# Performance work log

Measured on AMD Instinct MI355X. Metric: run time of the kernel, lower is better.

The kernel has to match this reference:

```python
import jax, jax.numpy as jnp
import numpy as np

B, L, D = 2, 1024, 1024
H = 16
NL = 2
DFF = 4 * D
EPS = 1e-5
W_SCALE = 0.02


def rmsnorm(x, w):
    # x * rsqrt(mean(x^2, -1) + eps) * w   (computed in fp32 as in the torch code)
    xf = x.astype(jnp.float32)
    n = xf * jax.lax.rsqrt(jnp.mean(xf * xf, axis=-1, keepdims=True) + EPS)
    return n.astype(x.dtype) * w


def setup_inputs() -> dict:
    key = jax.random.key(0)
    ks = jax.random.split(key, 10)
    x = jax.random.normal(ks[0], (B, L, D), dtype=jnp.float32)
    # torch nn.Linear weight layout: [out_features, in_features]; y = x @ W.T + b
    qw = jax.random.normal(ks[1], (NL, D, D), dtype=jnp.float32) * W_SCALE
    kw = jax.random.normal(ks[2], (NL, D, D), dtype=jnp.float32) * W_SCALE
    vw = jax.random.normal(ks[3], (NL, D, D), dtype=jnp.float32) * W_SCALE
    ow = jax.random.normal(ks[4], (NL, D, D), dtype=jnp.float32) * W_SCALE
    pn_w = jnp.ones((NL, D), dtype=jnp.float32)
    ln_w = jnp.ones((NL, D), dtype=jnp.float32)
    fc_w = jax.random.normal(ks[5], (NL, DFF, D), dtype=jnp.float32) * W_SCALE
    fc2_w = jax.random.normal(ks[6], (NL, D, DFF), dtype=jnp.float32) * W_SCALE
    fc2_b = jnp.zeros((NL, D), dtype=jnp.float32)
    return {"x": x, "qw": qw, "kw": kw, "vw": vw, "ow": ow,
            "pn_w": pn_w, "ln_w": ln_w, "fc_w": fc_w, "fc2_w": fc2_w, "fc2_b": fc2_b}


def reference(x, qw, kw, vw, ow, pn_w, ln_w, fc_w, fc2_w, fc2_b):
    d = D // H
    for i in range(NL):
        # --- LinearAttention block (dropout=0 -> identity) ---
        h = rmsnorm(x, pn_w[i])                                   # [B,L,D]
        Q = (h @ qw[i].T).reshape(B, L, H, d)
        K = (h @ kw[i].T).reshape(B, L, H, d)
        V = (h @ vw[i].T).reshape(B, L, H, d)
        # outer-product state per position, cumulated over L (causal linear attn)
        W = jnp.einsum('blhd,blhe->blhde', K, V)                  # [B,L,H,d,d]
        W = jnp.cumsum(W, axis=1)
        a = jnp.einsum('blhd,blhde->blhe', Q, W).reshape(B, L, D)
        x = x + a @ ow[i].T
        # --- MLP block ---
        m = rmsnorm(x, ln_w[i])
        f = jax.nn.gelu(m @ fc_w[i].T, approximate=False)         # torch nn.GELU default = exact
        x = x + f @ fc2_w[i].T + fc2_b[i]
    return x
```

## Files before the change

kernel.cpp:

```cpp
#include <hip/hip_runtime.h>

#define BB 2
#define LL 1024
#define DD 1024
#define HH 16
#define HD 64
#define DFFN 4096
#define MM (BB*LL)
#define QS 3072

using u16 = unsigned short;
typedef __bf16 bf16x8 __attribute__((ext_vector_type(8)));
typedef float f32x4 __attribute__((ext_vector_type(4)));

__device__ __forceinline__ float b2f(u16 u) {
  union { unsigned int i; float f; } v; v.i = ((unsigned int)u) << 16; return v.f;
}
__device__ __forceinline__ u16 f2b(float f) {
  union { float f; unsigned int i; } v; v.f = f;
  unsigned int x = v.i;
  return (u16)((x + 0x7fffu + ((x >> 16) & 1u)) >> 16);
}
__device__ __forceinline__ float gelu_exact(float x) {
  return 0.5f * x * (1.0f + erff(x * 0.70710678118654752f));
}
__device__ __forceinline__ void gl2lds16(const void* g, void* l) {
  __builtin_amdgcn_global_load_lds((const __attribute__((address_space(1))) void*)g,
                                   (__attribute__((address_space(3))) void*)l, 16, 0, 0);
}

__global__ __launch_bounds__(256) void castw_kernel(const float* __restrict__ in,
                                                    u16* __restrict__ out, int n8) {
  int i = blockIdx.x * 256 + threadIdx.x;
  if (i >= n8) return;
  const float4 a = reinterpret_cast<const float4*>(in)[2 * i];
  const float4 b = reinterpret_cast<const float4*>(in)[2 * i + 1];
  uint4 o;
  o.x = (unsigned)f2b(a.x) | ((unsigned)f2b(a.y) << 16);
  o.y = (unsigned)f2b(a.z) | ((unsigned)f2b(a.w) << 16);
  o.z = (unsigned)f2b(b.x) | ((unsigned)f2b(b.y) << 16);
  o.w = (unsigned)f2b(b.z) | ((unsigned)f2b(b.w) << 16);
  reinterpret_cast<uint4*>(out)[i] = o;
}

__global__ __launch_bounds__(256) void rmsnorm_kernel(const float* __restrict__ x,
                                                      const float* __restrict__ w,
                                                      u16* __restrict__ out) {
  const int row = blockIdx.x, t = threadIdx.x;
  const float4 v = reinterpret_cast<const float4*>(x + (size_t)row * DD)[t];
  float ss = v.x*v.x + v.y*v.y + v.z*v.z + v.w*v.w;
  #pragma unroll
  for (int o = 32; o > 0; o >>= 1) ss += __shfl_down(ss, o);
  __shared__ float red[4];
  if ((t & 63) == 0) red[t >> 6] = ss;
  __syncthreads();
  const float inv = rsqrtf((red[0] + red[1] + red[2] + red[3]) * (1.0f / DD) + 1e-5f);
  const float4 wv = reinterpret_cast<const float4*>(w)[t];
  ushort4 o;
  o.x = f2b(v.x * inv * wv.x);
  o.y = f2b(v.y * inv * wv.y);
  o.z = f2b(v.z * inv * wv.z);
  o.w = f2b(v.w * inv * wv.w);
  reinterpret_cast<ushort4*>(out + (size_t)row * DD)[t] = o;
}

template<int BM, int BN, int ACT, int RES>
__global__ __launch_bounds__((BM/64)*(BN/64)*64)
void mfma_gemm(const u16* __restrict__ A, const u16* __restrict__ Wb,
               u16* __restrict__ Cb, const float* __restrict__ resid,
               float* __restrict__ Co, const float* __restrict__ bias,
               int N, int K) {
  constexpr int WCOLS = BN / 64;
  constexpr int NW = (BM / 64) * WCOLS;
  constexpr int NT = NW * 64;
  constexpr int CA = BM * 4;
  constexpr int CB = BN * 4;
  constexpr int IA = CA / NT, IB = CB / NT;
  __shared__ u16 As[BM * 32];
  __shared__ u16 Bs[BN * 32];
  const int t = threadIdx.x;
  const int lane = t & 63, w = t >> 6;
  const int wm = (w / WCOLS) * 64, wn = (w % WCOLS) * 64;
  const int m0 = blockIdx.y * BM, n0 = blockIdx.x * BN;
  const int fr = lane & 15, fq = lane >> 4;

  f32x4 acc[4][4] = {};

  for (int kt = 0; kt < K; kt += 32) {
    #pragma unroll
    for (int i = 0; i < IA; i++) {
      const int c = i * NT + t;
      gl2lds16(A + (size_t)(m0 + (c >> 2)) * K + kt + (c & 3) * 8, &As[c * 8]);
    }
    #pragma unroll
    for (int i = 0; i < IB; i++) {
      const int c = i * NT + t;
      gl2lds16(Wb + (size_t)(n0 + (c >> 2)) * K + kt + (c & 3) * 8, &Bs[c * 8]);
    }
    __syncthreads();
    bf16x8 af[4], bfv[4];
    #pragma unroll
    for (int i = 0; i < 4; i++)
      af[i] = *reinterpret_cast<const bf16x8*>(&As[(wm + i * 16 + fr) * 32 + fq * 8]);
    #pragma unroll
    for (int j = 0; j < 4; j++)
      bfv[j] = *reinterpret_cast<const bf16x8*>(&Bs[(wn + j * 16 + fr) * 32 + fq * 8]);
    #pragma unroll
    for (int i = 0; i < 4; i++)
      #pragma unroll
      for (int j = 0; j < 4; j++)
        acc[i][j] = __builtin_amdgcn_mfma_f32_16x16x32_bf16(af[i], bfv[j], acc[i][j], 0, 0, 0);
    __syncthreads();
  }

  #pragma unroll
  for (int i = 0; i < 4; i++) {
    #pragma unroll
    for (int j = 0; j < 4; j++) {
      #pragma unroll
      for (int r = 0; r < 4; r++) {
        const int row = m0 + wm + i * 16 + fq * 4 + r;
        const int col = n0 + wn + j * 16 + fr;
        float val = acc[i][j][r];
        if (RES == 0) {
          if (ACT == 1) val = gelu_exact(val);
          Cb[(size_t)row * N + col] = f2b(val);
        } else {
          const float rv = resid[(size_t)row * N + col];
          const float bv = (bias != nullptr) ? bias[col] : 0.0f;
          Co[(size_t)row * N + col] = rv + val + bv;
        }
      }
    }
  }
}

__global__ __launch_bounds__(256) void kv_trans(const u16* __restrict__ QKV,
                                                u16* __restrict__ Kt, u16* __restrict__ Vt) {
  const int tile = blockIdx.x;
  const int h2 = blockIdx.y;
  const int b = blockIdx.z;
  const int h = h2 & 15, which = h2 >> 4;
  const int t = threadIdx.x;
  const int pos = tile * 64 + (t >> 2), d0 = (t & 3) * 16;
  const u16* src = QKV + ((size_t)(b * LL) + pos) * QS + 1024 + which * 1024 + h * HD + d0;
  union { uint4 u[2]; u16 s[16]; } pk;
  pk.u[0] = reinterpret_cast<const uint4*>(src)[0];
  pk.u[1] = reinterpret_cast<const uint4*>(src)[1];
  u16* dst = (which ? Vt : Kt) + ((size_t)(b * HH + h) * HD + d0) * LL + pos;
  #pragma unroll
  for (int j = 0; j < 16; j++) dst[(size_t)j * LL] = pk.s[j];
}

__global__ __launch_bounds__(256) void attn_phase1(const u16* __restrict__ QKV,
                                                   const u16* __restrict__ Kt,
                                                   const u16* __restrict__ Vt,
                                                   u16* __restrict__ Oa,
                                                   u16* __restrict__ Slt) {
  __shared__ u16 Ss[4][16][64];
  const int tile = blockIdx.x, h = blockIdx.y, b = blockIdx.z;
  const int t = threadIdx.x, lane = t & 63, w = t >> 6;
  const int fr = lane & 15, fq = lane >> 4;
  const size_t tok0 = (size_t)(b * LL + tile * 64);
  const size_t bh = (size_t)(b * HH + h);
  const u16* Qb  = QKV + tok0 * QS + h * HD;
  const u16* Kb  = Qb + 1024;
  const u16* Ktb = Kt + bh * (HD * LL) + tile * 64;
  const u16* Vtb = Vt + bh * (HD * LL) + tile * 64;

  bf16x8 aq[2], bk[4][2];
  #pragma unroll
  for (int kh = 0; kh < 2; kh++)
    aq[kh] = *reinterpret_cast<const bf16x8*>(Qb + (size_t)(16*w + fr) * QS + kh*32 + fq*8);
  #pragma unroll
  for (int n4 = 0; n4 < 4; n4++)
    #pragma unroll
    for (int kh = 0; kh < 2; kh++)
      bk[n4][kh] = *reinterpret_cast<const bf16x8*>(Kb + (size_t)(16*n4 + fr) * QS + kh*32 + fq*8);
  f32x4 sacc[4] = {};
  #pragma unroll
  for (int n4 = 0; n4 < 4; n4++) {
    sacc[n4] = __builtin_amdgcn_mfma_f32_16x16x32_bf16(aq[0], bk[n4][0], sacc[n4], 0, 0, 0);
    sacc[n4] = __builtin_amdgcn_mfma_f32_16x16x32_bf16(aq[1], bk[n4][1], sacc[n4], 0, 0, 0);
  }
  #pragma unroll
  for (int n4 = 0; n4 < 4; n4++)
    #pragma unroll
    for (int r = 0; r < 4; r++) {
      const bool keep = (16*w + 4*fq + r) >= (16*n4 + fr);
      Ss[w][4*fq + r][16*n4 + fr] = keep ? f2b(sacc[n4][r]) : (u16)0;
    }
  __syncthreads();

  bf16x8 va[2], kt[4][2];
  #pragma unroll
  for (int kh = 0; kh < 2; kh++)
    va[kh] = *reinterpret_cast<const bf16x8*>(Vtb + (size_t)(16*w + fr) * LL + kh*32 + fq*8);
  #pragma unroll
  for (int n4 = 0; n4 < 4; n4++)
    #pragma unroll
    for (int kh = 0; kh < 2; kh++)
      kt[n4][kh] = *reinterpret_cast<const bf16x8*>(Ktb + (size_t)(16*n4 + fr) * LL + kh*32 + fq*8);
  f32x4 lacc[4] = {};
  #pragma unroll
  for (int n4 = 0; n4 < 4; n4++) {
    lacc[n4] = __builtin_amdgcn_mfma_f32_16x16x32_bf16(va[0], kt[n4][0], lacc[n4], 0, 0, 0);
    lacc[n4] = __builtin_amdgcn_mfma_f32_16x16x32_bf16(va[1], kt[n4][1], lacc[n4], 0, 0, 0);
  }
  u16* So = Slt + (bh * 16 + tile) * 4096;
  #pragma unroll
  for (int n4 = 0; n4 < 4; n4++)
    #pragma unroll
    for (int r = 0; r < 4; r++)
      So[(size_t)(16*w + 4*fq + r) * 64 + 16*n4 + fr] = f2b(lacc[n4][r]);

  bf16x8 sa[2], vb[4][2];
  #pragma unroll
  for (int kh = 0; kh < 2; kh++)
    sa[kh] = *reinterpret_cast<const bf16x8*>(&Ss[w][fr][kh*32 + fq*8]);
  #pragma unroll
  for (int n4 = 0; n4 < 4; n4++)
    #pragma unroll
    for (int kh = 0; kh < 2; kh++)
      vb[n4][kh] = *reinterpret_cast<const bf16x8*>(Vtb + (size_t)(16*n4 + fr) * LL + kh*32 + fq*8);
  f32x4 oacc[4] = {};
  #pragma unroll
  for (int n4 = 0; n4 < 4; n4++) {
    oacc[n4] = __builtin_amdgcn_mfma_f32_16x16x32_bf16(sa[0], vb[n4][0], oacc[n4], 0, 0, 0);
    oacc[n4] = __builtin_amdgcn_mfma_f32_16x16x32_bf16(sa[1], vb[n4][1], oacc[n4], 0, 0, 0);
  }
  u16* Ob = Oa + (tok0 + 16*w) * DD + h * HD;
  #pragma unroll
  for (int n4 = 0; n4 < 4; n4++)
    #pragma unroll
    for (int r = 0; r < 4; r++)
      Ob[(size_t)(4*fq + r) * DD + 16*n4 + fr] = f2b(oacc[n4][r]);
}

__global__ __launch_bounds__(256) void attn_phase2(const u16* __restrict__ Slt,
                                                   u16* __restrict__ Wc) {
  const int rg = blockIdx.x, h = blockIdx.y, b = blockIdx.z;
  const size_t base = ((size_t)((b * HH + h) * 16)) * 4096 + rg * 512 + threadIdx.x * 2;
  float r0 = 0.f, r1 = 0.f;
  for (int tl = 0; tl < 16; tl++) {
    const size_t p = base + (size_t)tl * 4096;
    const unsigned d = *reinterpret_cast<const unsigned*>(Slt + p);
    *reinterpret_cast<unsigned*>(Wc + p) = (unsigned)f2b(r0) | ((unsigned)f2b(r1) << 16);
    r0 += b2f((u16)(d & 0xffff));
    r1 += b2f((u16)(d >> 16));
  }
}

__global__ __launch_bounds__(256) void attn_phase3(const u16* __restrict__ QKV,
                                                   const u16* __restrict__ Wc,
                                                   u16* __restrict__ Oa) {
  const int tile = blockIdx.x, h = blockIdx.y, b = blockIdx.z;
  const int t = threadIdx.x, lane = t & 63, w = t >> 6;
  const int fr = lane & 15, fq = lane >> 4;
  const size_t tok0 = (size_t)(b * LL + tile * 64);
  const size_t bh = (size_t)(b * HH + h);
  const u16* Qb = QKV + tok0 * QS + h * HD;
  const u16* Wb = Wc + (bh * 16 + tile) * 4096;

  bf16x8 aq[2], wb[4][2];
  #pragma unroll
  for (int kh = 0; kh < 2; kh++)
    aq[kh] = *reinterpret_cast<const bf16x8*>(Qb + (size_t)(16*w + fr) * QS + kh*32 + fq*8);
  #pragma unroll
  for (int n4 = 0; n4 < 4; n4++)
    #pragma unroll
    for (int kh = 0; kh < 2; kh++)
      wb[n4][kh] = *reinterpret_cast<const bf16x8*>(Wb + (size_t)(16*n4 + fr) * 64 + kh*32 + fq*8);
  f32x4 oacc[4] = {};
  #pragma unroll
  for (int n4 = 0; n4 < 4; n4++) {
    oacc[n4] = __builtin_amdgcn_mfma_f32_16x16x32_bf16(aq[0], wb[n4][0], oacc[n4], 0, 0, 0);
    oacc[n4] = __builtin_amdgcn_mfma_f32_16x16x32_bf16(aq[1], wb[n4][1], oacc[n4], 0, 0, 0);
  }
  u16* Ob = Oa + (tok0 + 16*w) * DD + h * HD;
  #pragma unroll
  for (int n4 = 0; n4 < 4; n4++)
    #pragma unroll
    for (int r = 0; r < 4; r++) {
      const size_t idx = (size_t)(4*fq + r) * DD + 16*n4 + fr;
      Ob[idx] = f2b(b2f(Ob[idx]) + oacc[n4][r]);
    }
}

extern "C" void kernel_launch(void* const* d_in, const int* in_sizes, int n_in,
                              void* d_out, int out_size, void* d_ws, size_t ws_size,
                              hipStream_t stream) {
  const float* x_in = (const float*)d_in[0];
  const float* qw   = (const float*)d_in[1];
  const float* kw   = (const float*)d_in[2];
  const float* vw   = (const float*)d_in[3];
  const float* ow   = (const float*)d_in[4];
  const float* pn   = (const float*)d_in[5];
  const float* ln   = (const float*)d_in[6];
  const float* fcw  = (const float*)d_in[7];
  const float* fc2w = (const float*)d_in[8];
  const float* fc2b = (const float*)d_in[9];

  char* ws = (char*)d_ws;
  u16* wbuf = (u16*)ws;
  u16* slt  = (u16*)ws;
  u16* wcum = (u16*)(ws + (size_t)(4 << 20));
  u16* h    = (u16*)(ws + (size_t)(8 << 20));
  u16* qkv  = (u16*)(ws + (size_t)(12 << 20));
  u16* f    = (u16*)(ws + (size_t)(12 << 20));
  u16* vt   = (u16*)(ws + (size_t)(24 << 20));
  u16* kt   = (u16*)(ws + (size_t)(28 << 20));
  float* xf = (float*)d_out;

  const int n8D = DD * DD / 8;
  const int n8F = DFFN * DD / 8;

  for (int i = 0; i < 2; i++) {
    const float* qwi  = qw   + (size_t)i * DD * DD;
    const float* kwi  = kw   + (size_t)i * DD * DD;
    const float* vwi  = vw   + (size_t)i * DD * DD;
    const float* owi  = ow   + (size_t)i * DD * DD;
    const float* fcwi = fcw  + (size_t)i * DFFN * DD;
    const float* f2wi = fc2w + (size_t)i * DD * DFFN;
    const float* src  = (i == 0) ? x_in : xf;

    rmsnorm_kernel<<<MM, 256, 0, stream>>>(src, pn + i * DD, h);
    castw_kernel<<<n8D / 256, 256, 0, stream>>>(qwi, wbuf,               n8D);
    castw_kernel<<<n8D / 256, 256, 0, stream>>>(kwi, wbuf + DD * DD,     n8D);
    castw_kernel<<<n8D / 256, 256, 0, stream>>>(vwi, wbuf + 2 * DD * DD, n8D);
    mfma_gemm<128, 128, 0, 0><<<dim3(QS / 128, MM / 128), 256, 0, stream>>>(
        h, wbuf, qkv, nullptr, nullptr, nullptr, QS, DD);
    kv_trans<<<dim3(16, 32, BB), 256, 0, stream>>>(qkv, kt, vt);
    attn_phase1<<<dim3(16, HH, BB), 256, 0, stream>>>(qkv, kt, vt, h, slt);
    attn_phase2<<<dim3(8, HH, BB), 256, 0, stream>>>(slt, wcum);
    attn_phase3<<<dim3(16, HH, BB), 256, 0, stream>>>(qkv, wcum, h);
    castw_kernel<<<n8D / 256, 256, 0, stream>>>(owi, wbuf, n8D);
    mfma_gemm<64, 128, 0, 1><<<dim3(DD / 128, MM / 64), 128, 0, stream>>>(
        h, wbuf, nullptr, src, xf, nullptr, DD, DD);
    rmsnorm_kernel<<<MM, 256, 0, stream>>>(xf, ln + i * DD, h);
    castw_kernel<<<n8F / 256, 256, 0, stream>>>(fcwi, wbuf, n8F);
    mfma_gemm<128, 128, 1, 0><<<dim3(DFFN / 128, MM / 128), 256, 0, stream>>>(
        h, wbuf, f, nullptr, nullptr, nullptr, DFFN, DD);
    castw_kernel<<<n8F / 256, 256, 0, stream>>>(f2wi, wbuf, n8F);
    float* co = (i == 1) ? (float*)d_out : xf;
    mfma_gemm<64, 128, 0, 1><<<dim3(DD / 128, MM / 64), 128, 0, stream>>>(
        f, wbuf, nullptr, xf, co, fc2b + i * DD, DD, DFFN);
  }
}
```

Measured before the change: 607.1 us.

## Split-K residual GEMMs with atomics, fuse QKV weight casts, tile kv transpose

```diff
diff --git a/kernel.cpp b/kernel.cpp
--- a/kernel.cpp
+++ b/kernel.cpp
@@ -42,6 +42,35 @@
   o.w = (unsigned)f2b(b.z) | ((unsigned)f2b(b.w) << 16);
   reinterpret_cast<uint4*>(out)[i] = o;
 }
+__global__ __launch_bounds__(256) void castw3_kernel(const float* __restrict__ s0,
+                                                     const float* __restrict__ s1,
+                                                     const float* __restrict__ s2,
+                                                     u16* __restrict__ out, int n8) {
+  int i = blockIdx.x * 256 + threadIdx.x;
+  if (i >= n8) return;
+  const float* in = (blockIdx.y == 0) ? s0 : (blockIdx.y == 1) ? s1 : s2;
+  u16* dst = out + (size_t)blockIdx.y * n8 * 8;
+  const float4 a = reinterpret_cast<const float4*>(in)[2 * i];
+  const float4 b = reinterpret_cast<const float4*>(in)[2 * i + 1];
+  uint4 o;
+  o.x = (unsigned)f2b(a.x) | ((unsigned)f2b(a.y) << 16);
+  o.y = (unsigned)f2b(a.z) | ((unsigned)f2b(a.w) << 16);
+  o.z = (unsigned)f2b(b.x) | ((unsigned)f2b(b.y) << 16);
+  o.w = (unsigned)f2b(b.z) | ((unsigned)f2b(b.w) << 16);
+  reinterpret_cast<uint4*>(dst)[i] = o;
+}
+
+__global__ __launch_bounds__(256) void init_out_kernel(float* __restrict__ out,
+                                                       const float* __restrict__ resid,
+                                                       const float* __restrict__ bias) {
+  const int i = blockIdx.x * 256 + threadIdx.x;
+  float4 v = reinterpret_cast<const float4*>(resid)[i];
+  if (bias != nullptr) {
+    const float4 bv = *reinterpret_cast<const float4*>(bias + ((i * 4) & (DD - 1)));
+    v.x += bv.x; v.y += bv.y; v.z += bv.z; v.w += bv.w;
+  }
+  reinterpret_cast<float4*>(out)[i] = v;
+}
 
 __global__ __launch_bounds__(256) void rmsnorm_kernel(const float* __restrict__ x,
                                                       const float* __restrict__ w,
@@ -64,18 +93,14 @@
   reinterpret_cast<ushort4*>(out + (size_t)row * DD)[t] = o;
 }
 
-template<int BM, int BN, int ACT, int RES>
+template<int BM, int BN, int ACT>
 __global__ __launch_bounds__((BM/64)*(BN/64)*64)
 void mfma_gemm(const u16* __restrict__ A, const u16* __restrict__ Wb,
-               u16* __restrict__ Cb, const float* __restrict__ resid,
-               float* __restrict__ Co, const float* __restrict__ bias,
-               int N, int K) {
+               u16* __restrict__ Cb, int N, int K) {
   constexpr int WCOLS = BN / 64;
   constexpr int NW = (BM / 64) * WCOLS;
   constexpr int NT = NW * 64;
-  constexpr int CA = BM * 4;
-  constexpr int CB = BN * 4;
-  constexpr int IA = CA / NT, IB = CB / NT;
+  constexpr int IA = BM * 4 / NT, IB = BN * 4 / NT;
   __shared__ u16 As[BM * 32];
   __shared__ u16 Bs[BN * 32];
   const int t = threadIdx.x;
@@ -85,7 +110,6 @@
   const int fr = lane & 15, fq = lane >> 4;
 
   f32x4 acc[4][4] = {};
-
   for (int kt = 0; kt < K; kt += 32) {
     #pragma unroll
     for (int i = 0; i < IA; i++) {
@@ -114,42 +138,92 @@
   }
 
   #pragma unroll
-  for (int i = 0; i < 4; i++) {
-    #pragma unroll
-    for (int j = 0; j < 4; j++) {
+  for (int i = 0; i < 4; i++)
+    #pragma unroll
+    for (int j = 0; j < 4; j++)
       #pragma unroll
       for (int r = 0; r < 4; r++) {
         const int row = m0 + wm + i * 16 + fq * 4 + r;
         const int col = n0 + wn + j * 16 + fr;
         float val = acc[i][j][r];
-        if (RES == 0) {
-          if (ACT == 1) val = gelu_exact(val);
-          Cb[(size_t)row * N + col] = f2b(val);
-        } else {
-          const float rv = resid[(size_t)row * N + col];
-          const float bv = (bias != nullptr) ? bias[col] : 0.0f;
-          Co[(size_t)row * N + col] = rv + val + bv;
-        }
+        if (ACT == 1) val = gelu_exact(val);
+        Cb[(size_t)row * N + col] = f2b(val);
       }
+}
+
+template<int SPLIT>
+__global__ __launch_bounds__(256)
+void mfma_gemm_sk(const u16* __restrict__ A, const u16* __restrict__ Wb,
+                  float* __restrict__ Co, int N, int K) {
+  constexpr int BM = 128, BN = 128;
+  __shared__ u16 As[BM * 32];
+  __shared__ u16 Bs[BN * 32];
+  const int t = threadIdx.x;
+  const int lane = t & 63, w = t >> 6;
+  const int wm = (w >> 1) * 64, wn = (w & 1) * 64;
+  const int m0 = blockIdx.y * BM, n0 = blockIdx.x * BN;
+  const int fr = lane & 15, fq = lane >> 4;
+  const int Kc = K / SPLIT, k0 = blockIdx.z * Kc;
+
+  f32x4 acc[4][4] = {};
+  for (int kt = k0; kt < k0 + Kc; kt += 32) {
+    #pragma unroll
+    for (int i = 0; i < 2; i++) {
+      const int c = i * 256 + t;
+      gl2lds16(A + (size_t)(m0 + (c >> 2)) * K + kt + (c & 3) * 8, &As[c * 8]);
+      gl2lds16(Wb + (size_t)(n0 + (c >> 2)) * K + kt + (c & 3) * 8, &Bs[c * 8]);
     }
-  }
+    __syncthreads();
+    bf16x8 af[4], bfv[4];
+    #pragma unroll
+    for (int i = 0; i < 4; i++)
+      af[i] = *reinterpret_cast<const bf16x8*>(&As[(wm + i * 16 + fr) * 32 + fq * 8]);
+    #pragma unroll
+    for (int j = 0; j < 4; j++)
+      bfv[j] = *reinterpret_cast<const bf16x8*>(&Bs[(wn + j * 16 + fr) * 32 + fq * 8]);
+    #pragma unroll
+    for (int i = 0; i < 4; i++)
+      #pragma unroll
+      for (int j = 0; j < 4; j++)
+        acc[i][j] = __builtin_amdgcn_mfma_f32_16x16x32_bf16(af[i], bfv[j], acc[i][j], 0, 0, 0);
+    __syncthreads();
+  }
+
+  #pragma unroll
+  for (int i = 0; i < 4; i++)
+    #pragma unroll
+    for (int j = 0; j < 4; j++)
+      #pragma unroll
+      for (int r = 0; r < 4; r++) {
+        const int row = m0 + wm + i * 16 + fq * 4 + r;
+        const int col = n0 + wn + j * 16 + fr;
+        unsafeAtomicAdd(&Co[(size_t)row * N + col], acc[i][j][r]);
+      }
 }
 
 __global__ __launch_bounds__(256) void kv_trans(const u16* __restrict__ QKV,
                                                 u16* __restrict__ Kt, u16* __restrict__ Vt) {
+  __shared__ u16 T[64][72];
   const int tile = blockIdx.x;
   const int h2 = blockIdx.y;
   const int b = blockIdx.z;
   const int h = h2 & 15, which = h2 >> 4;
   const int t = threadIdx.x;
-  const int pos = tile * 64 + (t >> 2), d0 = (t & 3) * 16;
-  const u16* src = QKV + ((size_t)(b * LL) + pos) * QS + 1024 + which * 1024 + h * HD + d0;
+  const int pos = t >> 2, d0 = (t & 3) * 16;
+  const u16* src = QKV + ((size_t)(b * LL) + tile * 64 + pos) * QS + 1024 + which * 1024 + h * HD + d0;
   union { uint4 u[2]; u16 s[16]; } pk;
   pk.u[0] = reinterpret_cast<const uint4*>(src)[0];
   pk.u[1] = reinterpret_cast<const uint4*>(src)[1];
-  u16* dst = (which ? Vt : Kt) + ((size_t)(b * HH + h) * HD + d0) * LL + pos;
-  #pragma unroll
-  for (int j = 0; j < 16; j++) dst[(size_t)j * LL] = pk.s[j];
+  #pragma unroll
+  for (int j = 0; j < 16; j++) T[d0 + j][pos] = pk.s[j];
+  __syncthreads();
+  const int d = t >> 2, p0 = (t & 3) * 16;
+  u16* dst = (which ? Vt : Kt) + ((size_t)(b * HH + h) * HD + d) * LL + tile * 64 + p0;
+  union { uint4 u[2]; u16 s[16]; } ok;
+  #pragma unroll
+  for (int j = 0; j < 16; j++) ok.s[j] = T[d][p0 + j];
+  reinterpret_cast<uint4*>(dst)[0] = ok.u[0];
+  reinterpret_cast<uint4*>(dst)[1] = ok.u[1];
 }
 
 __global__ __launch_bounds__(256) void attn_phase1(const u16* __restrict__ QKV,
@@ -314,6 +388,7 @@
 
   const int n8D = DD * DD / 8;
   const int n8F = DFFN * DD / 8;
+  const int gInit = MM * DD / 4 / 256;
 
   for (int i = 0; i < 2; i++) {
     const float* qwi  = qw   + (size_t)i * DD * DD;
@@ -325,25 +400,23 @@
     const float* src  = (i == 0) ? x_in : xf;
 
     rmsnorm_kernel<<<MM, 256, 0, stream>>>(src, pn + i * DD, h);
-    castw_kernel<<<n8D / 256, 256, 0, stream>>>(qwi, wbuf,               n8D);
-    castw_kernel<<<n8D / 256, 256, 0, stream>>>(kwi, wbuf + DD * DD,     n8D);
-    castw_kernel<<<n8D / 256, 256, 0, stream>>>(vwi, wbuf + 2 * DD * DD, n8D);
-    mfma_gemm<128, 128, 0, 0><<<dim3(QS / 128, MM / 128), 256, 0, stream>>>(
-        h, wbuf, qkv, nullptr, nullptr, nullptr, QS, DD);
+    castw3_kernel<<<dim3(n8D / 256, 3), 256, 0, stream>>>(qwi, kwi, vwi, wbuf, n8D);
+    mfma_gemm<128, 128, 0><<<dim3(QS / 128, MM / 128), 256, 0, stream>>>(
+        h, wbuf, qkv, QS, DD);
     kv_trans<<<dim3(16, 32, BB), 256, 0, stream>>>(qkv, kt, vt);
     attn_phase1<<<dim3(16, HH, BB), 256, 0, stream>>>(qkv, kt, vt, h, slt);
     attn_phase2<<<dim3(8, HH, BB), 256, 0, stream>>>(slt, wcum);
     attn_phase3<<<dim3(16, HH, BB), 256, 0, stream>>>(qkv, wcum, h);
     castw_kernel<<<n8D / 256, 256, 0, stream>>>(owi, wbuf, n8D);
-    mfma_gemm<64, 128, 0, 1><<<dim3(DD / 128, MM / 64), 128, 0, stream>>>(
-        h, wbuf, nullptr, src, xf, nullptr, DD, DD);
+    init_out_kernel<<<gInit, 256, 0, stream>>>(xf, src, nullptr);
+    mfma_gemm_sk<4><<<dim3(DD / 128, MM / 128, 4), 256, 0, stream>>>(h, wbuf, xf, DD, DD);
     rmsnorm_kernel<<<MM, 256, 0, stream>>>(xf, ln + i * DD, h);
     castw_kernel<<<n8F / 256, 256, 0, stream>>>(fcwi, wbuf, n8F);
-    mfma_gemm<128, 128, 1, 0><<<dim3(DFFN / 128, MM / 128), 256, 0, stream>>>(
-        h, wbuf, f, nullptr, nullptr, nullptr, DFFN, DD);
+    mfma_gemm<128, 128, 1><<<dim3(DFFN / 128, MM / 128), 256, 0, stream>>>(
+        h, wbuf, f, DFFN, DD);
     castw_kernel<<<n8F / 256, 256, 0, stream>>>(f2wi, wbuf, n8F);
     float* co = (i == 1) ? (float*)d_out : xf;
-    mfma_gemm<64, 128, 0, 1><<<dim3(DD / 128, MM / 64), 128, 0, stream>>>(
-        f, wbuf, nullptr, xf, co, fc2b + i * DD, DD, DFFN);
-  }
-}
+    init_out_kernel<<<gInit, 256, 0, stream>>>(co, xf, fc2b + i * DD);
+    mfma_gemm_sk<4><<<dim3(DD / 128, MM / 128, 4), 256, 0, stream>>>(f, wbuf, co, DD, DFFN);
+  }
+}
```

Result: faster. 547.0 us (-9.9%).
